# Optimization experiments

Hardware: AMD Instinct MI355X
Metric: run time of the kernel (lower is better)

## Reference

```python
import jax, jax.numpy as jnp
import numpy as np

SCORE_THRESH = 0.05  # score_thresh arg of interaction_inference_single_image


def setup_inputs() -> dict:
    key = jax.random.key(0)
    ks = jax.random.split(key, 6)
    R, K = 262144, 117
    return {
        "person_boxes": jax.random.uniform(ks[0], (R, 4), dtype=jnp.float32) * 512.0,
        "object_boxes": jax.random.uniform(ks[1], (R, 4), dtype=jnp.float32) * 512.0,
        "person_box_scores": jax.random.uniform(ks[2], (R,), dtype=jnp.float32),
        "object_box_scores": jax.random.uniform(ks[3], (R,), dtype=jnp.float32),
        "object_box_classes": jax.random.randint(ks[4], (R, 1), 0, 80, dtype=jnp.int32),
        "hoi_scores": jax.random.uniform(ks[5], (R, K), dtype=jnp.float32),
        "topk_per_image": 100,
    }


def reference(person_boxes, object_boxes, person_box_scores, object_box_scores,
              object_box_classes, hoi_scores, topk_per_image):
    # scores[r, k] = hoi_scores[r, k] * person_score[r] * object_score[r]
    R, K = hoi_scores.shape
    box_scores = person_box_scores * object_box_scores          # (R,)
    scores = hoi_scores * box_scores[:, None]                    # (R, K)

    # Fused threshold + top-k: entries failing the threshold are pushed to -inf
    # so they can never enter the top-k; `valid` marks real detections.
    flat = scores.reshape(-1)                                    # (R*K,)
    masked = jnp.where(flat > SCORE_THRESH, flat, -jnp.inf)
    top_vals, top_idx = jax.lax.top_k(masked, topk_per_image)    # sorted descending
    valid = top_vals > SCORE_THRESH                              # (topk,) bool

    pair_idx = top_idx // K                                      # filter_inds[:, 0]
    action_classes = top_idx % K                                 # filter_inds[:, 1]

    out_scores = jnp.where(valid, top_vals, 0.0)
    out_person_boxes = person_boxes[pair_idx]                    # (topk, 4)
    out_object_boxes = object_boxes[pair_idx]                    # (topk, 4)
    out_object_classes = object_box_classes[pair_idx, 0]         # (topk,)
    return (out_scores, out_person_boxes, out_object_boxes,
            out_object_classes, action_classes, valid)
```

## Files before the change

### kernel.cpp

```cpp
#include <hip/hip_runtime.h>


#define NB        576
#define BIN_BASE  15692
#define WLO       500
#define WN        80
#define VLO       0.75f
#define G_REL     538
#define CAP       8192
#define FCAP      2048
#define THRESH    0.05f
#define NEG_INF   __int_as_float(0xFF800000)

__device__ __forceinline__ int bin_of(float s) {
  int b = (int)(__float_as_uint(s) >> 16) - BIN_BASE;
  return b > (NB - 1) ? (NB - 1) : b;
}

template <int KC>
__global__ __launch_bounds__(256) void k_hist(
    const float4* __restrict__ hoi4, const float* __restrict__ ps,
    const float* __restrict__ os, int N4, int N, int Kc,
    int* __restrict__ g_whist, int* __restrict__ g_cnt,
    float* __restrict__ cand_v, int* __restrict__ cand_i) {
  __shared__ int lh[WN];
  if (threadIdx.x < WN) lh[threadIdx.x] = 0;
  __syncthreads();

  const int k = KC ? KC : Kc;
  const int TT = gridDim.x * blockDim.x;
  const int tid = blockIdx.x * blockDim.x + threadIdx.x;

  auto process = [&](int t, float4 h) {
    int i0 = 4 * t;
    int q = i0 / k;
    int rem = i0 - q * k;
    float bsa = ps[q] * os[q];
    int qb = (rem + 3 >= k) ? q + 1 : q;
    float bsb = ps[qb] * os[qb];
    float vals[4] = {h.x, h.y, h.z, h.w};
#pragma unroll
    for (int j = 0; j < 4; ++j) {
      float bs = (rem + j >= k) ? bsb : bsa;
      float s = vals[j] * bs;
      if (s > VLO) {
        int b = bin_of(s);
        atomicAdd(&lh[b - WLO], 1);
        if (b >= G_REL) {
          int slot = atomicAdd(g_cnt, 1);
          if (slot < CAP) { cand_v[slot] = s; cand_i[slot] = i0 + j; }
        }
      }
    }
  };

  for (int t0 = tid; t0 < N4; t0 += 4 * TT) {
    int t1 = t0 + TT, t2 = t0 + 2 * TT, t3 = t0 + 3 * TT;
    float4 h0 = hoi4[t0];
    float4 h1 = hoi4[t1 < N4 ? t1 : t0];
    float4 h2 = hoi4[t2 < N4 ? t2 : t0];
    float4 h3 = hoi4[t3 < N4 ? t3 : t0];
    process(t0, h0);
    if (t1 < N4) process(t1, h1);
    if (t2 < N4) process(t2, h2);
    if (t3 < N4) process(t3, h3);
  }
  if (blockIdx.x == 0) {
    const float* hoi = (const float*)hoi4;
    for (int i = N4 * 4 + threadIdx.x; i < N; i += blockDim.x) {
      int q = i / k;
      float s = hoi[i] * (ps[q] * os[q]);
      if (s > VLO) {
        int b = bin_of(s);
        atomicAdd(&lh[b - WLO], 1);
        if (b >= G_REL) {
          int slot = atomicAdd(g_cnt, 1);
          if (slot < CAP) { cand_v[slot] = s; cand_i[slot] = i; }
        }
      }
    }
  }
  __syncthreads();
  if (threadIdx.x < WN) {
    int c = lh[threadIdx.x];
    if (c) atomicAdd(&g_whist[threadIdx.x], c);
  }
}

__global__ void k_thresh(const int* __restrict__ g_whist,
                         int* __restrict__ g_cnt, int* __restrict__ g_meta,
                         int topk) {
  __shared__ int wh[WN];
  if (threadIdx.x < WN) wh[threadIdx.x] = g_whist[threadIdx.x];
  __syncthreads();
  if (threadIdx.x == 0) {
    int cum = 0, T = -1;
#pragma unroll
    for (int b = WN - 1; b >= 0; --b) {
      cum += wh[b];
      if (T < 0 && cum >= topk) T = b + WLO;
    }
    int cnt = g_cnt[0];
    int fast = (T >= G_REL && cnt <= CAP) ? 1 : 0;
    g_meta[0] = T;
    g_meta[1] = fast ? 0 : 1;
    if (!fast) g_cnt[0] = 0;
  }
}

__global__ __launch_bounds__(1024) void k_fallback(
    const float* __restrict__ hoi, const float* __restrict__ ps,
    const float* __restrict__ os, int N, int Kc,
    int* __restrict__ g_meta, int* __restrict__ g_cnt,
    float* __restrict__ cand_v, int* __restrict__ cand_i, int topk) {
  if (g_meta[1] == 0) return;
  __shared__ int lh[NB];
  __shared__ int sT;
  for (int b = threadIdx.x; b < NB; b += blockDim.x) lh[b] = 0;
  __syncthreads();
  for (int i = threadIdx.x; i < N; i += blockDim.x) {
    int q = i / Kc;
    float s = hoi[i] * (ps[q] * os[q]);
    if (s > THRESH) atomicAdd(&lh[bin_of(s)], 1);
  }
  __syncthreads();
  if (threadIdx.x == 0) {
    int cum = 0, T = 0;
    for (int b = NB - 1; b >= 0; --b) {
      cum += lh[b];
      if (cum >= topk) { T = b; break; }
    }
    g_meta[0] = T;
    sT = T;
  }
  __syncthreads();
  const int T = sT;
  for (int i = threadIdx.x; i < N; i += blockDim.x) {
    int q = i / Kc;
    float s = hoi[i] * (ps[q] * os[q]);
    if (s > THRESH && bin_of(s) >= T) {
      int slot = atomicAdd(g_cnt, 1);
      if (slot < CAP) { cand_v[slot] = s; cand_i[slot] = i; }
    }
  }
}

__global__ __launch_bounds__(1024) void k_final(
    const float* __restrict__ cand_v, const int* __restrict__ cand_i,
    const int* __restrict__ g_cnt, const int* __restrict__ g_meta,
    const float4* __restrict__ pbox, const float4* __restrict__ obox,
    const int* __restrict__ ocls, float* __restrict__ out, int topk, int Kc) {
  __shared__ float sv[FCAP];
  __shared__ int si[FCAP];
  __shared__ int scnt;
  if (threadIdx.x == 0) scnt = 0;
  __syncthreads();

  const int T = g_meta[0];
  int n = g_cnt[0];
  if (n > CAP) n = CAP;
  for (int t = threadIdx.x; t < n; t += blockDim.x) {
    float v = cand_v[t];
    if (bin_of(v) >= T) {
      int slot = atomicAdd(&scnt, 1);
      if (slot < FCAP) { sv[slot] = v; si[slot] = cand_i[t]; }
    }
  }
  __syncthreads();
  int m = scnt > FCAP ? FCAP : scnt;
  int P = 128;
  while (P < m) P <<= 1;
  for (int t = threadIdx.x + m; t < P; t += blockDim.x) {
    sv[t] = NEG_INF;
    si[t] = 0x7FFFFFFF;
  }

  for (int kk = 2; kk <= P; kk <<= 1) {
    for (int j = kk >> 1; j > 0; j >>= 1) {
      __syncthreads();
      for (int i = threadIdx.x; i < P; i += blockDim.x) {
        int l = i ^ j;
        if (l > i) {
          float vi = sv[i], vl = sv[l];
          int ii = si[i], il = si[l];
          bool before = (vi > vl) || (vi == vl && ii < il);
          bool up = ((i & kk) == 0);
          if (up != before) { sv[i] = vl; sv[l] = vi; si[i] = il; si[l] = ii; }
        }
      }
    }
  }
  __syncthreads();

  if ((int)threadIdx.x < topk) {
    int o = threadIdx.x;
    float v = sv[o];
    int idx = si[o];
    bool valid = (idx != 0x7FFFFFFF) && (v > THRESH);
    int safe = valid ? idx : 0;
    int pair = safe / Kc;
    int act = safe - pair * Kc;
    float4 pb = pbox[pair];
    float4 ob = obox[pair];
    out[o] = valid ? v : 0.0f;
    float* pdst = out + topk + 4 * o;
    pdst[0] = pb.x; pdst[1] = pb.y; pdst[2] = pb.z; pdst[3] = pb.w;
    float* odst = out + 5 * topk + 4 * o;
    odst[0] = ob.x; odst[1] = ob.y; odst[2] = ob.z; odst[3] = ob.w;
    out[9 * topk + o] = (float)ocls[pair];
    out[10 * topk + o] = (float)act;
    out[11 * topk + o] = valid ? 1.0f : 0.0f;
  }
}

extern "C" void kernel_launch(void* const* d_in, const int* in_sizes, int n_in,
                              void* d_out, int out_size, void* d_ws, size_t ws_size,
                              hipStream_t stream) {
  const float* pbox = (const float*)d_in[0];
  const float* obox = (const float*)d_in[1];
  const float* ps   = (const float*)d_in[2];
  const float* os   = (const float*)d_in[3];
  const int*   ocls = (const int*)d_in[4];
  const float* hoi  = (const float*)d_in[5];
  float* out = (float*)d_out;

  const int R    = in_sizes[2];
  const int N    = in_sizes[5];
  const int Kc   = N / R;
  const int topk = out_size / 12;

  int* g_cnt   = (int*)d_ws;
  int* g_meta  = g_cnt + 1;
  int* g_whist = g_cnt + 8;
  float* cand_v = (float*)((char*)d_ws + 4096);
  int*   cand_i = (int*)((char*)d_ws + 4096 + CAP * sizeof(float));

  hipMemsetAsync(d_ws, 0, 4096, stream);

  const int N4 = N / 4;
  if (Kc == 117) {
    k_hist<117><<<2048, 256, 0, stream>>>((const float4*)hoi, ps, os, N4, N,
                                          Kc, g_whist, g_cnt, cand_v, cand_i);
  } else {
    k_hist<0><<<2048, 256, 0, stream>>>((const float4*)hoi, ps, os, N4, N, Kc,
                                        g_whist, g_cnt, cand_v, cand_i);
  }
  k_thresh<<<1, 128, 0, stream>>>(g_whist, g_cnt, g_meta, topk);
  k_fallback<<<1, 1024, 0, stream>>>(hoi, ps, os, N, Kc, g_meta, g_cnt,
                                     cand_v, cand_i, topk);
  k_final<<<1, 1024, 0, stream>>>(cand_v, cand_i, g_cnt, g_meta,
                                  (const float4*)pbox, (const float4*)obox,
                                  ocls, out, topk, Kc);
}
```

Measured before the change: 243.6 us.

## Fuse threshold and final sort into histogram kernel via last-block pattern

Merges the histogram, threshold, and final sort/gather stages into one kernel: the last block to finish, found with an atomic counter, sums the histogram and sorts the candidates. This removes two separate kernel launches. Block histograms are now accumulated into 32 replicated copies to reduce contention on the global atomics. Each element is first tested on its raw hoi value, so the person and object scores are only loaded and multiplied when that value already exceeds the cutoff. In exchange, the serial sort runs on 256 threads instead of 1024, and every block reserves extra shared memory for the sort buffers, which may lower occupancy.

```diff
diff --git a/kernel.cpp b/kernel.cpp
--- a/kernel.cpp
+++ b/kernel.cpp
@@ -7,8 +7,9 @@
 #define WN        80
 #define VLO       0.75f
 #define G_REL     538
-#define CAP       8192
 #define FCAP      2048
+#define NREP      32
+#define REPS      96
 #define THRESH    0.05f
 #define NEG_INF   __int_as_float(0xFF800000)
 
@@ -17,13 +18,20 @@
   return b > (NB - 1) ? (NB - 1) : b;
 }
 
+
 template <int KC>
-__global__ __launch_bounds__(256) void k_hist(
+__global__ __launch_bounds__(256) void k_main(
     const float4* __restrict__ hoi4, const float* __restrict__ ps,
-    const float* __restrict__ os, int N4, int N, int Kc,
-    int* __restrict__ g_whist, int* __restrict__ g_cnt,
-    float* __restrict__ cand_v, int* __restrict__ cand_i) {
+    const float* __restrict__ os, const float4* __restrict__ pbox,
+    const float4* __restrict__ obox, const int* __restrict__ ocls,
+    int N4, int N, int Kc, int* __restrict__ ctrl, int* __restrict__ rep,
+    float* __restrict__ cand_v, int* __restrict__ cand_i, int cap,
+    float* __restrict__ out, int topk) {
   __shared__ int lh[WN];
+  __shared__ int wh[WN];
+  __shared__ float sv[FCAP];
+  __shared__ int si[FCAP];
+  __shared__ int s_misc[4];
   if (threadIdx.x < WN) lh[threadIdx.x] = 0;
   __syncthreads();
 
@@ -31,24 +39,22 @@
   const int TT = gridDim.x * blockDim.x;
   const int tid = blockIdx.x * blockDim.x + threadIdx.x;
 
-  auto process = [&](int t, float4 h) {
+  auto process = [&](int t, const float4& h) {
+    float vals[4] = {h.x, h.y, h.z, h.w};
     int i0 = 4 * t;
-    int q = i0 / k;
-    int rem = i0 - q * k;
-    float bsa = ps[q] * os[q];
-    int qb = (rem + 3 >= k) ? q + 1 : q;
-    float bsb = ps[qb] * os[qb];
-    float vals[4] = {h.x, h.y, h.z, h.w};
 #pragma unroll
     for (int j = 0; j < 4; ++j) {
-      float bs = (rem + j >= k) ? bsb : bsa;
-      float s = vals[j] * bs;
-      if (s > VLO) {
-        int b = bin_of(s);
-        atomicAdd(&lh[b - WLO], 1);
-        if (b >= G_REL) {
-          int slot = atomicAdd(g_cnt, 1);
-          if (slot < CAP) { cand_v[slot] = s; cand_i[slot] = i0 + j; }
+      if (vals[j] > VLO) {
+        int i = i0 + j;
+        int q = i / k;
+        float s = vals[j] * (ps[q] * os[q]);
+        if (s > VLO) {
+          int b = bin_of(s);
+          atomicAdd(&lh[b - WLO], 1);
+          if (b >= G_REL) {
+            int slot = atomicAdd(&ctrl[0], 1);
+            if (slot < cap) { cand_v[slot] = s; cand_i[slot] = i; }
+          }
         }
       }
     }
@@ -68,14 +74,17 @@
   if (blockIdx.x == 0) {
     const float* hoi = (const float*)hoi4;
     for (int i = N4 * 4 + threadIdx.x; i < N; i += blockDim.x) {
-      int q = i / k;
-      float s = hoi[i] * (ps[q] * os[q]);
-      if (s > VLO) {
-        int b = bin_of(s);
-        atomicAdd(&lh[b - WLO], 1);
-        if (b >= G_REL) {
-          int slot = atomicAdd(g_cnt, 1);
-          if (slot < CAP) { cand_v[slot] = s; cand_i[slot] = i; }
+      float v = hoi[i];
+      if (v > VLO) {
+        int q = i / k;
+        float s = v * (ps[q] * os[q]);
+        if (s > VLO) {
+          int b = bin_of(s);
+          atomicAdd(&lh[b - WLO], 1);
+          if (b >= G_REL) {
+            int slot = atomicAdd(&ctrl[0], 1);
+            if (slot < cap) { cand_v[slot] = s; cand_i[slot] = i; }
+          }
         }
       }
     }
@@ -83,98 +92,62 @@
   __syncthreads();
   if (threadIdx.x < WN) {
     int c = lh[threadIdx.x];
-    if (c) atomicAdd(&g_whist[threadIdx.x], c);
-  }
-}
-
-__global__ void k_thresh(const int* __restrict__ g_whist,
-                         int* __restrict__ g_cnt, int* __restrict__ g_meta,
-                         int topk) {
-  __shared__ int wh[WN];
-  if (threadIdx.x < WN) wh[threadIdx.x] = g_whist[threadIdx.x];
+    if (c) atomicAdd(&rep[(blockIdx.x & (NREP - 1)) * REPS + threadIdx.x], c);
+  }
+  __threadfence();
+  __syncthreads();
+  if (threadIdx.x == 0) {
+    int prev = atomicAdd(&ctrl[1], 1);
+    s_misc[0] = (prev == (int)gridDim.x - 1) ? 1 : 0;
+  }
+  __syncthreads();
+  if (!s_misc[0]) return;
+
+  __threadfence();
+  if (threadIdx.x < WN) {
+    int sum = 0;
+#pragma unroll
+    for (int r = 0; r < NREP; ++r) sum += rep[r * REPS + threadIdx.x];
+    wh[threadIdx.x] = sum;
+  }
   __syncthreads();
   if (threadIdx.x == 0) {
     int cum = 0, T = -1;
-#pragma unroll
     for (int b = WN - 1; b >= 0; --b) {
       cum += wh[b];
       if (T < 0 && cum >= topk) T = b + WLO;
     }
-    int cnt = g_cnt[0];
-    int fast = (T >= G_REL && cnt <= CAP) ? 1 : 0;
-    g_meta[0] = T;
-    g_meta[1] = fast ? 0 : 1;
-    if (!fast) g_cnt[0] = 0;
-  }
-}
-
-__global__ __launch_bounds__(1024) void k_fallback(
-    const float* __restrict__ hoi, const float* __restrict__ ps,
-    const float* __restrict__ os, int N, int Kc,
-    int* __restrict__ g_meta, int* __restrict__ g_cnt,
-    float* __restrict__ cand_v, int* __restrict__ cand_i, int topk) {
-  if (g_meta[1] == 0) return;
-  __shared__ int lh[NB];
-  __shared__ int sT;
-  for (int b = threadIdx.x; b < NB; b += blockDim.x) lh[b] = 0;
-  __syncthreads();
-  for (int i = threadIdx.x; i < N; i += blockDim.x) {
-    int q = i / Kc;
-    float s = hoi[i] * (ps[q] * os[q]);
-    if (s > THRESH) atomicAdd(&lh[bin_of(s)], 1);
-  }
-  __syncthreads();
-  if (threadIdx.x == 0) {
-    int cum = 0, T = 0;
-    for (int b = NB - 1; b >= 0; --b) {
-      cum += lh[b];
-      if (cum >= topk) { T = b; break; }
-    }
-    g_meta[0] = T;
-    sT = T;
-  }
-  __syncthreads();
-  const int T = sT;
-  for (int i = threadIdx.x; i < N; i += blockDim.x) {
-    int q = i / Kc;
-    float s = hoi[i] * (ps[q] * os[q]);
-    if (s > THRESH && bin_of(s) >= T) {
-      int slot = atomicAdd(g_cnt, 1);
-      if (slot < CAP) { cand_v[slot] = s; cand_i[slot] = i; }
-    }
-  }
-}
-
-__global__ __launch_bounds__(1024) void k_final(
-    const float* __restrict__ cand_v, const int* __restrict__ cand_i,
-    const int* __restrict__ g_cnt, const int* __restrict__ g_meta,
-    const float4* __restrict__ pbox, const float4* __restrict__ obox,
-    const int* __restrict__ ocls, float* __restrict__ out, int topk, int Kc) {
-  __shared__ float sv[FCAP];
-  __shared__ int si[FCAP];
-  __shared__ int scnt;
-  if (threadIdx.x == 0) scnt = 0;
-  __syncthreads();
-
-  const int T = g_meta[0];
-  int n = g_cnt[0];
-  if (n > CAP) n = CAP;
+    int cnt = ctrl[0];
+    int fast = (T >= G_REL && cnt <= cap) ? 1 : 0;
+    ctrl[2] = T;
+    ctrl[3] = fast ? 0 : 1;
+    s_misc[1] = fast ? T : -1;
+    s_misc[2] = cnt > cap ? cap : cnt;
+    s_misc[3] = 0;
+  }
+  __syncthreads();
+  const int T = s_misc[1];
+  if (T < 0) return;
+  const int n = s_misc[2];
   for (int t = threadIdx.x; t < n; t += blockDim.x) {
     float v = cand_v[t];
     if (bin_of(v) >= T) {
-      int slot = atomicAdd(&scnt, 1);
+      int slot = atomicAdd(&s_misc[3], 1);
       if (slot < FCAP) { sv[slot] = v; si[slot] = cand_i[t]; }
     }
   }
   __syncthreads();
-  int m = scnt > FCAP ? FCAP : scnt;
+  int m = s_misc[3];
+  if (m > FCAP) {
+    if (threadIdx.x == 0) ctrl[3] = 1;
+    return;
+  }
   int P = 128;
   while (P < m) P <<= 1;
-  for (int t = threadIdx.x + m; t < P; t += blockDim.x) {
+  for (int t = m + threadIdx.x; t < P; t += blockDim.x) {
     sv[t] = NEG_INF;
     si[t] = 0x7FFFFFFF;
   }
-
   for (int kk = 2; kk <= P; kk <<= 1) {
     for (int j = kk >> 1; j > 0; j >>= 1) {
       __syncthreads();
@@ -184,14 +157,14 @@
           float vi = sv[i], vl = sv[l];
           int ii = si[i], il = si[l];
           bool before = (vi > vl) || (vi == vl && ii < il);
-          bool up = ((i & kk) == 0);
-          if (up != before) { sv[i] = vl; sv[l] = vi; si[i] = il; si[l] = ii; }
+          if (((i & kk) == 0) != before) {
+            sv[i] = vl; sv[l] = vi; si[i] = il; si[l] = ii;
+          }
         }
       }
     }
   }
   __syncthreads();
-
   if ((int)threadIdx.x < topk) {
     int o = threadIdx.x;
     float v = sv[o];
@@ -213,6 +186,90 @@
   }
 }
 
+__global__ __launch_bounds__(1024) void k_safety(
+    const float* __restrict__ hoi, const float* __restrict__ ps,
+    const float* __restrict__ os, const float4* __restrict__ pbox,
+    const float4* __restrict__ obox, const int* __restrict__ ocls,
+    int N, int Kc, const int* __restrict__ ctrl, float* __restrict__ out,
+    int topk) {
+  if (ctrl[3] == 0) return;
+  __shared__ int lh[NB];
+  __shared__ float sv[FCAP];
+  __shared__ int si[FCAP];
+  __shared__ int sT, scnt;
+  for (int b = threadIdx.x; b < NB; b += blockDim.x) lh[b] = 0;
+  if (threadIdx.x == 0) scnt = 0;
+  __syncthreads();
+  for (int i = threadIdx.x; i < N; i += blockDim.x) {
+    int q = i / Kc;
+    float s = hoi[i] * (ps[q] * os[q]);
+    if (s > THRESH) atomicAdd(&lh[bin_of(s)], 1);
+  }
+  __syncthreads();
+  if (threadIdx.x == 0) {
+    int cum = 0, T = 0;
+    for (int b = NB - 1; b >= 0; --b) {
+      cum += lh[b];
+      if (cum >= topk) { T = b; break; }
+    }
+    sT = T;
+  }
+  __syncthreads();
+  const int T = sT;
+  for (int i = threadIdx.x; i < N; i += blockDim.x) {
+    int q = i / Kc;
+    float s = hoi[i] * (ps[q] * os[q]);
+    if (s > THRESH && bin_of(s) >= T) {
+      int slot = atomicAdd(&scnt, 1);
+      if (slot < FCAP) { sv[slot] = s; si[slot] = i; }
+    }
+  }
+  __syncthreads();
+  int m = scnt > FCAP ? FCAP : scnt;
+  int P = 128;
+  while (P < m) P <<= 1;
+  for (int t = m + threadIdx.x; t < P; t += blockDim.x) {
+    sv[t] = NEG_INF;
+    si[t] = 0x7FFFFFFF;
+  }
+  for (int kk = 2; kk <= P; kk <<= 1) {
+    for (int j = kk >> 1; j > 0; j >>= 1) {
+      __syncthreads();
+      for (int i = threadIdx.x; i < P; i += blockDim.x) {
+        int l = i ^ j;
+        if (l > i) {
+          float vi = sv[i], vl = sv[l];
+          int ii = si[i], il = si[l];
+          bool before = (vi > vl) || (vi == vl && ii < il);
+          if (((i & kk) == 0) != before) {
+            sv[i] = vl; sv[l] = vi; si[i] = il; si[l] = ii;
+          }
+        }
+      }
+    }
+  }
+  __syncthreads();
+  if ((int)threadIdx.x < topk) {
+    int o = threadIdx.x;
+    float v = sv[o];
+    int idx = si[o];
+    bool valid = (idx != 0x7FFFFFFF) && (v > THRESH);
+    int safe = valid ? idx : 0;
+    int pair = safe / Kc;
+    int act = safe - pair * Kc;
+    float4 pb = pbox[pair];
+    float4 ob = obox[pair];
+    out[o] = valid ? v : 0.0f;
+    float* pdst = out + topk + 4 * o;
+    pdst[0] = pb.x; pdst[1] = pb.y; pdst[2] = pb.z; pdst[3] = pb.w;
+    float* odst = out + 5 * topk + 4 * o;
+    odst[0] = ob.x; odst[1] = ob.y; odst[2] = ob.z; odst[3] = ob.w;
+    out[9 * topk + o] = (float)ocls[pair];
+    out[10 * topk + o] = (float)act;
+    out[11 * topk + o] = valid ? 1.0f : 0.0f;
+  }
+}
+
 extern "C" void kernel_launch(void* const* d_in, const int* in_sizes, int n_in,
                               void* d_out, int out_size, void* d_ws, size_t ws_size,
                               hipStream_t stream) {
@@ -229,26 +286,26 @@
   const int Kc   = N / R;
   const int topk = out_size / 12;
 
-  int* g_cnt   = (int*)d_ws;
-  int* g_meta  = g_cnt + 1;
-  int* g_whist = g_cnt + 8;
-  float* cand_v = (float*)((char*)d_ws + 4096);
-  int*   cand_i = (int*)((char*)d_ws + 4096 + CAP * sizeof(float));
-
-  hipMemsetAsync(d_ws, 0, 4096, stream);
+  int* ctrl = (int*)d_ws;
+  int* rep  = (int*)((char*)d_ws + 256);
+  float* cand_v = (float*)((char*)d_ws + 12544);
+  size_t cand_budget = (ws_size > 12544) ? (ws_size - 12544) / 8 : 1024;
+  int cap = cand_budget > 8192 ? 8192 : (int)cand_budget;
+  int* cand_i = (int*)((char*)d_ws + 12544 + (size_t)cap * sizeof(float));
+
+  hipMemsetAsync(d_ws, 0, 12544, stream);
 
   const int N4 = N / 4;
   if (Kc == 117) {
-    k_hist<117><<<2048, 256, 0, stream>>>((const float4*)hoi, ps, os, N4, N,
-                                          Kc, g_whist, g_cnt, cand_v, cand_i);
+    k_main<117><<<2048, 256, 0, stream>>>(
+        (const float4*)hoi, ps, os, (const float4*)pbox, (const float4*)obox,
+        ocls, N4, N, Kc, ctrl, rep, cand_v, cand_i, cap, out, topk);
   } else {
-    k_hist<0><<<2048, 256, 0, stream>>>((const float4*)hoi, ps, os, N4, N, Kc,
-                                        g_whist, g_cnt, cand_v, cand_i);
-  }
-  k_thresh<<<1, 128, 0, stream>>>(g_whist, g_cnt, g_meta, topk);
-  k_fallback<<<1, 1024, 0, stream>>>(hoi, ps, os, N, Kc, g_meta, g_cnt,
-                                     cand_v, cand_i, topk);
-  k_final<<<1, 1024, 0, stream>>>(cand_v, cand_i, g_cnt, g_meta,
-                                  (const float4*)pbox, (const float4*)obox,
-                                  ocls, out, topk, Kc);
+    k_main<0><<<2048, 256, 0, stream>>>(
+        (const float4*)hoi, ps, os, (const float4*)pbox, (const float4*)obox,
+        ocls, N4, N, Kc, ctrl, rep, cand_v, cand_i, cap, out, topk);
+  }
+  k_safety<<<1, 1024, 0, stream>>>(hoi, ps, os, (const float4*)pbox,
+                                   (const float4*)obox, ocls, N, Kc, ctrl,
+                                   out, topk);
 }
```

Result: slower. 390.9 us (+60.5%).

## Merge threshold, fallback and final kernels; replicate histogram; deepen load unroll

Applied to the files above, without the earlier changes.

Folds the threshold, fallback and final-sort kernels into one post kernel, cutting two kernel launches and their dependent global round-trips. The per-block window histogram is now spread over 32 replicated copies to reduce global atomic contention, and those copies are summed in the post kernel. The streaming loop issues 8 float4 loads per iteration instead of 4 to keep more memory requests in flight. The candidate capacity is now derived from the workspace size, and the memset grows to cover the replicas.

```diff
diff --git a/kernel.cpp b/kernel.cpp
--- a/kernel.cpp
+++ b/kernel.cpp
@@ -7,8 +7,10 @@
 #define WN        80
 #define VLO       0.75f
 #define G_REL     538
-#define CAP       8192
 #define FCAP      2048
+#define NREP      32
+#define REPS      96
+#define UNROLL    8
 #define THRESH    0.05f
 #define NEG_INF   __int_as_float(0xFF800000)
 
@@ -17,12 +19,13 @@
   return b > (NB - 1) ? (NB - 1) : b;
 }
 
+
 template <int KC>
-__global__ __launch_bounds__(256) void k_hist(
+__global__ __launch_bounds__(256) void k_main(
     const float4* __restrict__ hoi4, const float* __restrict__ ps,
     const float* __restrict__ os, int N4, int N, int Kc,
-    int* __restrict__ g_whist, int* __restrict__ g_cnt,
-    float* __restrict__ cand_v, int* __restrict__ cand_i) {
+    int* __restrict__ ctrl, int* __restrict__ rep,
+    float* __restrict__ cand_v, int* __restrict__ cand_i, int cap) {
   __shared__ int lh[WN];
   if (threadIdx.x < WN) lh[threadIdx.x] = 0;
   __syncthreads();
@@ -31,7 +34,7 @@
   const int TT = gridDim.x * blockDim.x;
   const int tid = blockIdx.x * blockDim.x + threadIdx.x;
 
-  auto process = [&](int t, float4 h) {
+  auto process = [&](int t, const float4& h) {
     int i0 = 4 * t;
     int q = i0 / k;
     int rem = i0 - q * k;
@@ -41,29 +44,30 @@
     float vals[4] = {h.x, h.y, h.z, h.w};
 #pragma unroll
     for (int j = 0; j < 4; ++j) {
-      float bs = (rem + j >= k) ? bsb : bsa;
-      float s = vals[j] * bs;
+      float s = vals[j] * ((rem + j >= k) ? bsb : bsa);
       if (s > VLO) {
         int b = bin_of(s);
         atomicAdd(&lh[b - WLO], 1);
         if (b >= G_REL) {
-          int slot = atomicAdd(g_cnt, 1);
-          if (slot < CAP) { cand_v[slot] = s; cand_i[slot] = i0 + j; }
+          int slot = atomicAdd(&ctrl[0], 1);
+          if (slot < cap) { cand_v[slot] = s; cand_i[slot] = i0 + j; }
         }
       }
     }
   };
 
-  for (int t0 = tid; t0 < N4; t0 += 4 * TT) {
-    int t1 = t0 + TT, t2 = t0 + 2 * TT, t3 = t0 + 3 * TT;
-    float4 h0 = hoi4[t0];
-    float4 h1 = hoi4[t1 < N4 ? t1 : t0];
-    float4 h2 = hoi4[t2 < N4 ? t2 : t0];
-    float4 h3 = hoi4[t3 < N4 ? t3 : t0];
-    process(t0, h0);
-    if (t1 < N4) process(t1, h1);
-    if (t2 < N4) process(t2, h2);
-    if (t3 < N4) process(t3, h3);
+  for (int t0 = tid; t0 < N4; t0 += UNROLL * TT) {
+    float4 h[UNROLL];
+#pragma unroll
+    for (int j = 0; j < UNROLL; ++j) {
+      int t = t0 + j * TT;
+      h[j] = hoi4[t < N4 ? t : t0];
+    }
+#pragma unroll
+    for (int j = 0; j < UNROLL; ++j) {
+      int t = t0 + j * TT;
+      if (t < N4) process(t, h[j]);
+    }
   }
   if (blockIdx.x == 0) {
     const float* hoi = (const float*)hoi4;
@@ -74,8 +78,8 @@
         int b = bin_of(s);
         atomicAdd(&lh[b - WLO], 1);
         if (b >= G_REL) {
-          int slot = atomicAdd(g_cnt, 1);
-          if (slot < CAP) { cand_v[slot] = s; cand_i[slot] = i; }
+          int slot = atomicAdd(&ctrl[0], 1);
+          if (slot < cap) { cand_v[slot] = s; cand_i[slot] = i; }
         }
       }
     }
@@ -83,98 +87,89 @@
   __syncthreads();
   if (threadIdx.x < WN) {
     int c = lh[threadIdx.x];
-    if (c) atomicAdd(&g_whist[threadIdx.x], c);
-  }
-}
-
-__global__ void k_thresh(const int* __restrict__ g_whist,
-                         int* __restrict__ g_cnt, int* __restrict__ g_meta,
-                         int topk) {
-  __shared__ int wh[WN];
-  if (threadIdx.x < WN) wh[threadIdx.x] = g_whist[threadIdx.x];
+    if (c) atomicAdd(&rep[(blockIdx.x & (NREP - 1)) * REPS + threadIdx.x], c);
+  }
+}
+
+__global__ __launch_bounds__(1024) void k_post(
+    const float* __restrict__ hoi, const float* __restrict__ ps,
+    const float* __restrict__ os, const float4* __restrict__ pbox,
+    const float4* __restrict__ obox, const int* __restrict__ ocls,
+    int N, int Kc, const int* __restrict__ ctrl, const int* __restrict__ rep,
+    const float* __restrict__ cand_v, const int* __restrict__ cand_i,
+    int cap, float* __restrict__ out, int topk) {
+  __shared__ int wh[NB];
+  __shared__ float sv[FCAP];
+  __shared__ int si[FCAP];
+  __shared__ int s_T, s_n, s_cnt, s_mode;
+
+  if (threadIdx.x < WN) {
+    int sum = 0;
+#pragma unroll
+    for (int r = 0; r < NREP; ++r) sum += rep[r * REPS + threadIdx.x];
+    wh[threadIdx.x] = sum;
+  }
   __syncthreads();
   if (threadIdx.x == 0) {
     int cum = 0, T = -1;
-#pragma unroll
     for (int b = WN - 1; b >= 0; --b) {
       cum += wh[b];
       if (T < 0 && cum >= topk) T = b + WLO;
     }
-    int cnt = g_cnt[0];
-    int fast = (T >= G_REL && cnt <= CAP) ? 1 : 0;
-    g_meta[0] = T;
-    g_meta[1] = fast ? 0 : 1;
-    if (!fast) g_cnt[0] = 0;
-  }
-}
-
-__global__ __launch_bounds__(1024) void k_fallback(
-    const float* __restrict__ hoi, const float* __restrict__ ps,
-    const float* __restrict__ os, int N, int Kc,
-    int* __restrict__ g_meta, int* __restrict__ g_cnt,
-    float* __restrict__ cand_v, int* __restrict__ cand_i, int topk) {
-  if (g_meta[1] == 0) return;
-  __shared__ int lh[NB];
-  __shared__ int sT;
-  for (int b = threadIdx.x; b < NB; b += blockDim.x) lh[b] = 0;
-  __syncthreads();
-  for (int i = threadIdx.x; i < N; i += blockDim.x) {
-    int q = i / Kc;
-    float s = hoi[i] * (ps[q] * os[q]);
-    if (s > THRESH) atomicAdd(&lh[bin_of(s)], 1);
-  }
-  __syncthreads();
-  if (threadIdx.x == 0) {
-    int cum = 0, T = 0;
-    for (int b = NB - 1; b >= 0; --b) {
-      cum += lh[b];
-      if (cum >= topk) { T = b; break; }
-    }
-    g_meta[0] = T;
-    sT = T;
-  }
-  __syncthreads();
-  const int T = sT;
-  for (int i = threadIdx.x; i < N; i += blockDim.x) {
-    int q = i / Kc;
-    float s = hoi[i] * (ps[q] * os[q]);
-    if (s > THRESH && bin_of(s) >= T) {
-      int slot = atomicAdd(g_cnt, 1);
-      if (slot < CAP) { cand_v[slot] = s; cand_i[slot] = i; }
-    }
-  }
-}
-
-__global__ __launch_bounds__(1024) void k_final(
-    const float* __restrict__ cand_v, const int* __restrict__ cand_i,
-    const int* __restrict__ g_cnt, const int* __restrict__ g_meta,
-    const float4* __restrict__ pbox, const float4* __restrict__ obox,
-    const int* __restrict__ ocls, float* __restrict__ out, int topk, int Kc) {
-  __shared__ float sv[FCAP];
-  __shared__ int si[FCAP];
-  __shared__ int scnt;
-  if (threadIdx.x == 0) scnt = 0;
-  __syncthreads();
-
-  const int T = g_meta[0];
-  int n = g_cnt[0];
-  if (n > CAP) n = CAP;
-  for (int t = threadIdx.x; t < n; t += blockDim.x) {
-    float v = cand_v[t];
-    if (bin_of(v) >= T) {
-      int slot = atomicAdd(&scnt, 1);
-      if (slot < FCAP) { sv[slot] = v; si[slot] = cand_i[t]; }
-    }
-  }
-  __syncthreads();
-  int m = scnt > FCAP ? FCAP : scnt;
+    int cnt = ctrl[0];
+    s_mode = (T >= G_REL && cnt <= cap) ? 1 : 0;
+    s_T = T;
+    s_n = cnt > cap ? cap : cnt;
+    s_cnt = 0;
+  }
+  __syncthreads();
+
+  if (s_mode) {
+    const int T = s_T, n = s_n;
+    for (int t = threadIdx.x; t < n; t += blockDim.x) {
+      float v = cand_v[t];
+      if (bin_of(v) >= T) {
+        int slot = atomicAdd(&s_cnt, 1);
+        if (slot < FCAP) { sv[slot] = v; si[slot] = cand_i[t]; }
+      }
+    }
+  } else {
+    for (int b = threadIdx.x; b < NB; b += blockDim.x) wh[b] = 0;
+    __syncthreads();
+    for (int i = threadIdx.x; i < N; i += blockDim.x) {
+      int q = i / Kc;
+      float s = hoi[i] * (ps[q] * os[q]);
+      if (s > THRESH) atomicAdd(&wh[bin_of(s)], 1);
+    }
+    __syncthreads();
+    if (threadIdx.x == 0) {
+      int cum = 0, T = 0;
+      for (int b = NB - 1; b >= 0; --b) {
+        cum += wh[b];
+        if (cum >= topk) { T = b; break; }
+      }
+      s_T = T;
+    }
+    __syncthreads();
+    const int T = s_T;
+    for (int i = threadIdx.x; i < N; i += blockDim.x) {
+      int q = i / Kc;
+      float s = hoi[i] * (ps[q] * os[q]);
+      if (s > THRESH && bin_of(s) >= T) {
+        int slot = atomicAdd(&s_cnt, 1);
+        if (slot < FCAP) { sv[slot] = s; si[slot] = i; }
+      }
+    }
+  }
+  __syncthreads();
+
+  int m = s_cnt > FCAP ? FCAP : s_cnt;
   int P = 128;
   while (P < m) P <<= 1;
-  for (int t = threadIdx.x + m; t < P; t += blockDim.x) {
+  for (int t = m + threadIdx.x; t < P; t += blockDim.x) {
     sv[t] = NEG_INF;
     si[t] = 0x7FFFFFFF;
   }
-
   for (int kk = 2; kk <= P; kk <<= 1) {
     for (int j = kk >> 1; j > 0; j >>= 1) {
       __syncthreads();
@@ -184,8 +179,9 @@
           float vi = sv[i], vl = sv[l];
           int ii = si[i], il = si[l];
           bool before = (vi > vl) || (vi == vl && ii < il);
-          bool up = ((i & kk) == 0);
-          if (up != before) { sv[i] = vl; sv[l] = vi; si[i] = il; si[l] = ii; }
+          if (((i & kk) == 0) != before) {
+            sv[i] = vl; sv[l] = vi; si[i] = il; si[l] = ii;
+          }
         }
       }
     }
@@ -229,26 +225,24 @@
   const int Kc   = N / R;
   const int topk = out_size / 12;
 
-  int* g_cnt   = (int*)d_ws;
-  int* g_meta  = g_cnt + 1;
-  int* g_whist = g_cnt + 8;
-  float* cand_v = (float*)((char*)d_ws + 4096);
-  int*   cand_i = (int*)((char*)d_ws + 4096 + CAP * sizeof(float));
-
-  hipMemsetAsync(d_ws, 0, 4096, stream);
+  int* ctrl = (int*)d_ws;
+  int* rep  = (int*)((char*)d_ws + 256);
+  float* cand_v = (float*)((char*)d_ws + 12544);
+  size_t cand_budget = (ws_size > 12544) ? (ws_size - 12544) / 8 : 1024;
+  int cap = cand_budget > 8192 ? 8192 : (int)cand_budget;
+  int* cand_i = (int*)((char*)d_ws + 12544 + (size_t)cap * sizeof(float));
+
+  hipMemsetAsync(d_ws, 0, 12544, stream);
 
   const int N4 = N / 4;
   if (Kc == 117) {
-    k_hist<117><<<2048, 256, 0, stream>>>((const float4*)hoi, ps, os, N4, N,
-                                          Kc, g_whist, g_cnt, cand_v, cand_i);
+    k_main<117><<<2048, 256, 0, stream>>>((const float4*)hoi, ps, os, N4, N,
+                                          Kc, ctrl, rep, cand_v, cand_i, cap);
   } else {
-    k_hist<0><<<2048, 256, 0, stream>>>((const float4*)hoi, ps, os, N4, N, Kc,
-                                        g_whist, g_cnt, cand_v, cand_i);
-  }
-  k_thresh<<<1, 128, 0, stream>>>(g_whist, g_cnt, g_meta, topk);
-  k_fallback<<<1, 1024, 0, stream>>>(hoi, ps, os, N, Kc, g_meta, g_cnt,
-                                     cand_v, cand_i, topk);
-  k_final<<<1, 1024, 0, stream>>>(cand_v, cand_i, g_cnt, g_meta,
-                                  (const float4*)pbox, (const float4*)obox,
-                                  ocls, out, topk, Kc);
-}
+    k_main<0><<<2048, 256, 0, stream>>>((const float4*)hoi, ps, os, N4, N, Kc,
+                                        ctrl, rep, cand_v, cand_i, cap);
+  }
+  k_post<<<1, 1024, 0, stream>>>(hoi, ps, os, (const float4*)pbox,
+                                 (const float4*)obox, ocls, N, Kc, ctrl, rep,
+                                 cand_v, cand_i, cap, out, topk);
+}
```

Measured after the change: 222.0 us. 1.1x faster.
